# Kernel optimization log

Measured on AMD Instinct MI355X. Metric: run time of the kernel, lower is better.

The kernel has to match this reference:

```python
import jax, jax.numpy as jnp
import numpy as np

N, T, n, C, C2 = 4, 8, 16384, 64, 64

def setup_inputs() -> dict:
    key = jax.random.key(0)
    k1, k2, k3, k4, k5 = jax.random.split(key, 5)
    return {
        "key_mem": jax.random.normal(k1, (N, T, n, C), dtype=jnp.float32),
        "val_mem": jax.random.normal(k2, (N, T, n, C2), dtype=jnp.float32),
        "key_cur": jax.random.normal(k3, (N, n, C), dtype=jnp.float32),
        "val_cur": jax.random.normal(k4, (N, n, C2), dtype=jnp.float32),
        "alpha": jax.random.normal(k5, (1,), dtype=jnp.float32),
    }

def reference(key_mem, val_mem, key_cur, val_cur, alpha):
    # kv_mul: contract memory tokens (T*n) -> (N, C, C2), tiny matrix
    kv_mul = jnp.einsum('btnc,btnd->bcd', key_mem, val_mem)
    # softmax over the C axis (dim=1 in torch layout (N, C, C2))
    kv_mul = jax.nn.softmax(kv_mul, axis=1)
    # out: (N, n, C) @ (N, C, C2) -> (N, n, C2)
    out = jnp.einsum('bnc,bcd->bnd', key_cur, kv_mul)
    return alpha * out + val_cur
```

## Files before the change

kernel.cpp:

```cpp
#include <hip/hip_runtime.h>
#include <math.h>

#define N_TOK   16384
#define K_TOT   (8 * N_TOK)
#define N_BATCH 4
#define BPB     128
#define RPB     (K_TOT / BPB)
#define CHUNK   64
#define NCH     (RPB / CHUNK)
#define PITCH_U 34
#define PART_U  (64 * PITCH_U)

typedef short short8 __attribute__((ext_vector_type(8)));
typedef float f32x4  __attribute__((ext_vector_type(4)));

union FragU { uint4 u; short8 s; };

__device__ __forceinline__ uint bf16_rne(float f, float* rounded) {
  uint u = __float_as_uint(f);
  uint r = u + 0x7FFFu + ((u >> 16) & 1u);
  *rounded = __uint_as_float(r & 0xFFFF0000u);
  return r >> 16;
}

__device__ __forceinline__ void barrier_nodrain() {
  asm volatile("" ::: "memory");
  __builtin_amdgcn_s_waitcnt(0xC07F);
  __builtin_amdgcn_s_barrier();
  asm volatile("" ::: "memory");
}

__global__ __launch_bounds__(512, 2) void k1_mfma(
    const float* __restrict__ key, const float* __restrict__ val,
    float* __restrict__ part) {
  __shared__ uint lds[2][4 * PART_U];

  int blk  = blockIdx.x;
  int b    = blk / BPB;
  int p    = blk % BPB;
  int t    = threadIdx.x;
  int wave = t >> 6;
  int lane = t & 63;

  int arr = t >> 8;
  int tt  = t & 255;
  int c0  = (tt & 15) * 4;
  int r0  = (tt >> 4) * 4;
  const float* src = arr ? val : key;
  size_t rowbase = (size_t)b * K_TOT + (size_t)p * RPB;
  uint sbase = arr * 2 * PART_U;

  int mt  = wave >> 1;
  int ntb = (wave & 1) * 2;
  int m16 = lane & 15;
  int ko  = lane >> 4;

  f32x4 acc[2] = {{0.f, 0.f, 0.f, 0.f}, {0.f, 0.f, 0.f, 0.f}};
  float4 ld[2][4];

  auto load_chunk = [&](int ch, int par) {
#pragma unroll
    for (int q = 0; q < 4; q++)
      ld[par][q] =
          *(const float4*)&src[(rowbase + (size_t)ch * CHUNK + r0 + q) * 64 + c0];
  };

  auto write_chunk = [&](int par) {
#pragma unroll
    for (int cc = 0; cc < 4; cc++) {
      uint h[4], l[4];
#pragma unroll
      for (int q = 0; q < 4; q++) {
        float f = (&ld[par][q].x)[cc];
        float hf;
        h[q] = bf16_rne(f, &hf);
        float dummy;
        l[q] = bf16_rne(f - hf, &dummy);
      }
      uint2 hp = make_uint2(h[0] | (h[1] << 16), h[2] | (h[3] << 16));
      uint2 lp = make_uint2(l[0] | (l[1] << 16), l[2] | (l[3] << 16));
      uint base = sbase + (uint)(c0 + cc) * PITCH_U + (uint)(r0 >> 1);
      *(uint2*)&lds[par][base]          = hp;
      *(uint2*)&lds[par][base + PART_U] = lp;
    }
  };

  auto frag = [&](uint idx) {
    FragU F;
    uint2 a0 = *(const uint2*)&lds[0][0];
    (void)a0;
    uint2 lo = *(const uint2*)&((&lds[0][0])[idx]);
    uint2 hi = *(const uint2*)&((&lds[0][0])[idx + 2]);
    F.u = make_uint4(lo.x, lo.y, hi.x, hi.y);
    return F;
  };

  auto compute = [&](int par) {
    const uint* L = &lds[par][0];
#pragma unroll
    for (int ks = 0; ks < 2; ks++) {
      uint ao = (uint)(mt * 16 + m16) * PITCH_U + ks * 16 + ko * 4;
      FragU Ah, Al;
      {
        uint2 lo = *(const uint2*)&L[ao];
        uint2 hi = *(const uint2*)&L[ao + 2];
        Ah.u = make_uint4(lo.x, lo.y, hi.x, hi.y);
      }
      {
        uint2 lo = *(const uint2*)&L[ao + PART_U];
        uint2 hi = *(const uint2*)&L[ao + PART_U + 2];
        Al.u = make_uint4(lo.x, lo.y, hi.x, hi.y);
      }
#pragma unroll
      for (int nn = 0; nn < 2; nn++) {
        uint bo = 2 * PART_U + (uint)((ntb + nn) * 16 + m16) * PITCH_U +
                  ks * 16 + ko * 4;
        FragU Bh, Bl;
        {
          uint2 lo = *(const uint2*)&L[bo];
          uint2 hi = *(const uint2*)&L[bo + 2];
          Bh.u = make_uint4(lo.x, lo.y, hi.x, hi.y);
        }
        {
          uint2 lo = *(const uint2*)&L[bo + PART_U];
          uint2 hi = *(const uint2*)&L[bo + PART_U + 2];
          Bl.u = make_uint4(lo.x, lo.y, hi.x, hi.y);
        }
        acc[nn] = __builtin_amdgcn_mfma_f32_16x16x32_bf16(Ah.s, Bh.s, acc[nn], 0, 0, 0);
        acc[nn] = __builtin_amdgcn_mfma_f32_16x16x32_bf16(Ah.s, Bl.s, acc[nn], 0, 0, 0);
        acc[nn] = __builtin_amdgcn_mfma_f32_16x16x32_bf16(Al.s, Bh.s, acc[nn], 0, 0, 0);
      }
    }
  };

  load_chunk(0, 0);
  load_chunk(1, 1);
  write_chunk(0);
  barrier_nodrain();

#pragma unroll
  for (int ch = 0; ch < NCH; ch++) {
    if (ch + 2 < NCH) load_chunk(ch + 2, ch & 1);
    compute(ch & 1);
    if (ch + 1 < NCH) write_chunk((ch + 1) & 1);
    barrier_nodrain();
  }

  float* dst = part + (size_t)blk * 4096;
#pragma unroll
  for (int nn = 0; nn < 2; nn++) {
    int d = (ntb + nn) * 16 + m16;
#pragma unroll
    for (int r = 0; r < 4; r++) {
      int c = mt * 16 + ko * 4 + r;
      dst[c * 64 + d] = acc[nn][r];
    }
  }
}

__global__ __launch_bounds__(256, 4) void k2_reduce(
    const float* __restrict__ part, float* __restrict__ kv, int bpb) {
  int b  = blockIdx.x >> 6;
  int c  = blockIdx.x & 63;
  int p4 = threadIdx.x >> 6;
  int d  = threadIdx.x & 63;

  float s = 0.f;
  int iters = bpb >> 2;
  const float* src = part + (size_t)(b * bpb) * 4096 + c * 64 + d;
#pragma unroll 4
  for (int x = 0; x < iters; x++) s += src[(size_t)(p4 + 4 * x) * 4096];

  __shared__ float l[256];
  l[threadIdx.x] = s;
  __syncthreads();
  if (p4 == 0)
    kv[((size_t)b * 64 + c) * 64 + d] = l[d] + l[64 + d] + l[128 + d] + l[192 + d];
}

__global__ __launch_bounds__(256, 4) void k3_out(
    const float* __restrict__ kv, const float* __restrict__ keyc,
    const float* __restrict__ valc, const float* __restrict__ alphap,
    float* __restrict__ out) {
  __shared__ float Ps[4096];
  __shared__ float kT[64 * 68];
  __shared__ float redm[4][64];
  __shared__ float reds[4][64];

  int bb = blockIdx.x >> 8;
  int mb = blockIdx.x & 255;
  int m0 = mb * 64;
  int t = threadIdx.x;

  int d  = t & 63;
  int cg = t >> 6;
  const float* kvb = kv + (size_t)bb * 4096;
  float v[16];
  float mx = -3.0e38f;
#pragma unroll
  for (int i = 0; i < 16; i++) {
    v[i] = kvb[(cg * 16 + i) * 64 + d];
    mx = fmaxf(mx, v[i]);
  }
  redm[cg][d] = mx;

  int r  = t >> 2;
  int cb = (t & 3) * 16;
  const float* krow = keyc + ((size_t)bb * N_TOK + m0 + r) * 64;
#pragma unroll
  for (int u = 0; u < 4; u++) {
    float4 kk = *(const float4*)&krow[cb + 4 * u];
    int c = cb + 4 * u;
    kT[(c + 0) * 68 + r] = kk.x;
    kT[(c + 1) * 68 + r] = kk.y;
    kT[(c + 2) * 68 + r] = kk.z;
    kT[(c + 3) * 68 + r] = kk.w;
  }
  __syncthreads();

  mx = fmaxf(fmaxf(redm[0][d], redm[1][d]), fmaxf(redm[2][d], redm[3][d]));
  float s = 0.f;
#pragma unroll
  for (int i = 0; i < 16; i++) {
    float e = __expf(v[i] - mx);
    Ps[(cg * 16 + i) * 64 + d] = e;
    s += e;
  }
  reds[cg][d] = s;
  __syncthreads();

  int wave = t >> 6, lane = t & 63;
  int mi = lane >> 3, j = lane & 7;
  int m = wave * 16 + mi * 2;

  float acc[2][8];
#pragma unroll
  for (int a = 0; a < 2; a++)
#pragma unroll
    for (int dd = 0; dd < 8; dd++) acc[a][dd] = 0.f;

#pragma unroll 4
  for (int c = 0; c < 64; c++) {
    float2 kk = *(const float2*)&kT[c * 68 + m];
    float4 p0 = *(const float4*)&Ps[c * 64 + 8 * j];
    float4 p1 = *(const float4*)&Ps[c * 64 + 8 * j + 4];
    float pr[8] = {p0.x, p0.y, p0.z, p0.w, p1.x, p1.y, p1.z, p1.w};
#pragma unroll
    for (int dd = 0; dd < 8; dd++) {
      acc[0][dd] = fmaf(kk.x, pr[dd], acc[0][dd]);
      acc[1][dd] = fmaf(kk.y, pr[dd], acc[1][dd]);
    }
  }

  float alpha = alphap[0];
  float sc[8];
#pragma unroll
  for (int dd = 0; dd < 8; dd++) {
    int dq = 8 * j + dd;
    float den = reds[0][dq] + reds[1][dq] + reds[2][dq] + reds[3][dq];
    sc[dd] = alpha / den;
  }

#pragma unroll
  for (int a = 0; a < 2; a++) {
    size_t off = ((size_t)bb * N_TOK + m0 + m + a) * 64 + 8 * j;
    float4 v0 = *(const float4*)&valc[off];
    float4 v1 = *(const float4*)&valc[off + 4];
    float4 o0 = make_float4(fmaf(sc[0], acc[a][0], v0.x),
                            fmaf(sc[1], acc[a][1], v0.y),
                            fmaf(sc[2], acc[a][2], v0.z),
                            fmaf(sc[3], acc[a][3], v0.w));
    float4 o1 = make_float4(fmaf(sc[4], acc[a][4], v1.x),
                            fmaf(sc[5], acc[a][5], v1.y),
                            fmaf(sc[6], acc[a][6], v1.z),
                            fmaf(sc[7], acc[a][7], v1.w));
    *(float4*)&out[off] = o0;
    *(float4*)&out[off + 4] = o1;
  }
}

extern "C" void kernel_launch(void* const* d_in, const int* in_sizes, int n_in,
                              void* d_out, int out_size, void* d_ws,
                              size_t ws_size, hipStream_t stream) {
  const float* key_mem = (const float*)d_in[0];
  const float* val_mem = (const float*)d_in[1];
  const float* key_cur = (const float*)d_in[2];
  const float* val_cur = (const float*)d_in[3];
  const float* alpha   = (const float*)d_in[4];
  float* out = (float*)d_out;
  float* ws  = (float*)d_ws;

  float* part = ws;
  float* kv   = ws + (size_t)(N_BATCH * BPB) * 4096;

  k1_mfma<<<N_BATCH * BPB, 512, 0, stream>>>(key_mem, val_mem, part);
  k2_reduce<<<256, 256, 0, stream>>>(part, kv, BPB);
  k3_out<<<N_BATCH * (N_TOK / 64), 256, 0, stream>>>(kv, key_cur, val_cur,
                                                     alpha, out);
}
```

Before: 314.9 us.

## Replace split-bf16 MFMA reduction with fp32 FMA outer products fed by direct global-to-LDS loads

The first kernel stops converting key/value chunks to hi/lo bf16 pairs and running three MFMAs per tile. It now stages raw fp32 chunks straight into LDS with global_load_lds and accumulates 4x4 outer products with scalar FMAs, with the two half-blocks combined through LDS at the end. This drops the register round-trip and conversion work and gives exact fp32 accumulation, but moves the math from matrix cores to vector ALUs. The pipeline also shrinks from two chunks in flight to one.

```diff
diff --git a/kernel.cpp b/kernel.cpp
--- a/kernel.cpp
+++ b/kernel.cpp
@@ -8,32 +8,23 @@
 #define RPB     (K_TOT / BPB)
 #define CHUNK   64
 #define NCH     (RPB / CHUNK)
-#define PITCH_U 34
-#define PART_U  (64 * PITCH_U)
-
-typedef short short8 __attribute__((ext_vector_type(8)));
-typedef float f32x4  __attribute__((ext_vector_type(4)));
-
-union FragU { uint4 u; short8 s; };
-
-__device__ __forceinline__ uint bf16_rne(float f, float* rounded) {
-  uint u = __float_as_uint(f);
-  uint r = u + 0x7FFFu + ((u >> 16) & 1u);
-  *rounded = __uint_as_float(r & 0xFFFF0000u);
-  return r >> 16;
-}
-
-__device__ __forceinline__ void barrier_nodrain() {
-  asm volatile("" ::: "memory");
-  __builtin_amdgcn_s_waitcnt(0xC07F);
-  __builtin_amdgcn_s_barrier();
-  asm volatile("" ::: "memory");
-}
-
-__global__ __launch_bounds__(512, 2) void k1_mfma(
+
+
+typedef float f32x4 __attribute__((ext_vector_type(4)));
+
+__device__ __forceinline__ void gload16(const float* g, float* l) {
+  __builtin_amdgcn_global_load_lds(
+      (const __attribute__((address_space(1))) void*)g,
+      (__attribute__((address_space(3))) void*)l, 16, 0, 0);
+}
+
+#define WAIT_VM0   0x0F70u
+#define WAIT_LGKM0 0xC07Fu
+
+__global__ __launch_bounds__(512, 2) void k1_outer(
     const float* __restrict__ key, const float* __restrict__ val,
     float* __restrict__ part) {
-  __shared__ uint lds[2][4 * PART_U];
+  __shared__ float lds[2][8192];
 
   int blk  = blockIdx.x;
   int b    = blk / BPB;
@@ -42,118 +33,82 @@
   int wave = t >> 6;
   int lane = t & 63;
 
-  int arr = t >> 8;
-  int tt  = t & 255;
-  int c0  = (tt & 15) * 4;
-  int r0  = (tt >> 4) * 4;
-  const float* src = arr ? val : key;
-  size_t rowbase = (size_t)b * K_TOT + (size_t)p * RPB;
-  uint sbase = arr * 2 * PART_U;
-
-  int mt  = wave >> 1;
-  int ntb = (wave & 1) * 2;
-  int m16 = lane & 15;
-  int ko  = lane >> 4;
-
-  f32x4 acc[2] = {{0.f, 0.f, 0.f, 0.f}, {0.f, 0.f, 0.f, 0.f}};
-  float4 ld[2][4];
-
-  auto load_chunk = [&](int ch, int par) {
+  size_t base = ((size_t)b * K_TOT + (size_t)p * RPB) * 64;
+
+  const float* sarr = (wave < 4) ? (key + base) : (val + base);
+  uint ldsarr = (wave < 4) ? 0u : 4096u;
+  uint uoff   = (uint)((wave & 3) * 1024);
+
+  int half = t >> 8;
+  int tid  = t & 255;
+  int c4   = tid >> 4;
+  int d4   = tid & 15;
+  int r0   = half * 32;
+
+  float acc[4][4];
+#pragma unroll
+  for (int i = 0; i < 4; i++)
+#pragma unroll
+    for (int j = 0; j < 4; j++) acc[i][j] = 0.f;
+
+  auto stage = [&](int ch, int par) {
+    const float* g = sarr + (size_t)ch * (CHUNK * 64) + uoff + lane * 4;
+    float* l = &lds[par][ldsarr + uoff];
 #pragma unroll
     for (int q = 0; q < 4; q++)
-      ld[par][q] =
-          *(const float4*)&src[(rowbase + (size_t)ch * CHUNK + r0 + q) * 64 + c0];
+      gload16(g + q * 256, l + q * 256);
   };
 
-  auto write_chunk = [&](int par) {
-#pragma unroll
-    for (int cc = 0; cc < 4; cc++) {
-      uint h[4], l[4];
-#pragma unroll
-      for (int q = 0; q < 4; q++) {
-        float f = (&ld[par][q].x)[cc];
-        float hf;
-        h[q] = bf16_rne(f, &hf);
-        float dummy;
-        l[q] = bf16_rne(f - hf, &dummy);
-      }
-      uint2 hp = make_uint2(h[0] | (h[1] << 16), h[2] | (h[3] << 16));
-      uint2 lp = make_uint2(l[0] | (l[1] << 16), l[2] | (l[3] << 16));
-      uint base = sbase + (uint)(c0 + cc) * PITCH_U + (uint)(r0 >> 1);
-      *(uint2*)&lds[par][base]          = hp;
-      *(uint2*)&lds[par][base + PART_U] = lp;
+  auto compute = [&](int par) {
+    const float* Kb = &lds[par][(r0 << 6) + c4 * 4];
+    const float* Vb = &lds[par][4096 + (r0 << 6) + d4 * 4];
+#pragma unroll
+    for (int r = 0; r < 32; r++) {
+      float4 kk = *(const float4*)&Kb[r * 64];
+      float4 vv = *(const float4*)&Vb[r * 64];
+#pragma unroll
+      for (int i = 0; i < 4; i++)
+#pragma unroll
+        for (int j = 0; j < 4; j++)
+          acc[i][j] = fmaf((&kk.x)[i], (&vv.x)[j], acc[i][j]);
     }
   };
 
-  auto frag = [&](uint idx) {
-    FragU F;
-    uint2 a0 = *(const uint2*)&lds[0][0];
-    (void)a0;
-    uint2 lo = *(const uint2*)&((&lds[0][0])[idx]);
-    uint2 hi = *(const uint2*)&((&lds[0][0])[idx + 2]);
-    F.u = make_uint4(lo.x, lo.y, hi.x, hi.y);
-    return F;
-  };
-
-  auto compute = [&](int par) {
-    const uint* L = &lds[par][0];
-#pragma unroll
-    for (int ks = 0; ks < 2; ks++) {
-      uint ao = (uint)(mt * 16 + m16) * PITCH_U + ks * 16 + ko * 4;
-      FragU Ah, Al;
-      {
-        uint2 lo = *(const uint2*)&L[ao];
-        uint2 hi = *(const uint2*)&L[ao + 2];
-        Ah.u = make_uint4(lo.x, lo.y, hi.x, hi.y);
-      }
-      {
-        uint2 lo = *(const uint2*)&L[ao + PART_U];
-        uint2 hi = *(const uint2*)&L[ao + PART_U + 2];
-        Al.u = make_uint4(lo.x, lo.y, hi.x, hi.y);
-      }
-#pragma unroll
-      for (int nn = 0; nn < 2; nn++) {
-        uint bo = 2 * PART_U + (uint)((ntb + nn) * 16 + m16) * PITCH_U +
-                  ks * 16 + ko * 4;
-        FragU Bh, Bl;
-        {
-          uint2 lo = *(const uint2*)&L[bo];
-          uint2 hi = *(const uint2*)&L[bo + 2];
-          Bh.u = make_uint4(lo.x, lo.y, hi.x, hi.y);
-        }
-        {
-          uint2 lo = *(const uint2*)&L[bo + PART_U];
-          uint2 hi = *(const uint2*)&L[bo + PART_U + 2];
-          Bl.u = make_uint4(lo.x, lo.y, hi.x, hi.y);
-        }
-        acc[nn] = __builtin_amdgcn_mfma_f32_16x16x32_bf16(Ah.s, Bh.s, acc[nn], 0, 0, 0);
-        acc[nn] = __builtin_amdgcn_mfma_f32_16x16x32_bf16(Ah.s, Bl.s, acc[nn], 0, 0, 0);
-        acc[nn] = __builtin_amdgcn_mfma_f32_16x16x32_bf16(Al.s, Bh.s, acc[nn], 0, 0, 0);
-      }
-    }
-  };
-
-  load_chunk(0, 0);
-  load_chunk(1, 1);
-  write_chunk(0);
-  barrier_nodrain();
-
-#pragma unroll
+  stage(0, 0);
+  asm volatile("" ::: "memory");
+  __builtin_amdgcn_s_waitcnt(WAIT_VM0);
+  __builtin_amdgcn_s_barrier();
+  asm volatile("" ::: "memory");
+
+#pragma unroll 2
   for (int ch = 0; ch < NCH; ch++) {
-    if (ch + 2 < NCH) load_chunk(ch + 2, ch & 1);
+    if (ch + 1 < NCH) stage(ch + 1, (ch + 1) & 1);
     compute(ch & 1);
-    if (ch + 1 < NCH) write_chunk((ch + 1) & 1);
-    barrier_nodrain();
-  }
-
-  float* dst = part + (size_t)blk * 4096;
-#pragma unroll
-  for (int nn = 0; nn < 2; nn++) {
-    int d = (ntb + nn) * 16 + m16;
-#pragma unroll
-    for (int r = 0; r < 4; r++) {
-      int c = mt * 16 + ko * 4 + r;
-      dst[c * 64 + d] = acc[nn][r];
+    asm volatile("" ::: "memory");
+    __builtin_amdgcn_s_waitcnt(WAIT_VM0);
+    __builtin_amdgcn_s_barrier();
+    asm volatile("" ::: "memory");
+  }
+
+  float* scratch = &lds[0][0];
+  if (half) {
+#pragma unroll
+    for (int i = 0; i < 4; i++)
+      *(float4*)&scratch[tid * 20 + i * 4] =
+          make_float4(acc[i][0], acc[i][1], acc[i][2], acc[i][3]);
+  }
+  asm volatile("" ::: "memory");
+  __builtin_amdgcn_s_waitcnt(WAIT_LGKM0);
+  __builtin_amdgcn_s_barrier();
+  asm volatile("" ::: "memory");
+  if (!half) {
+    float* dst = part + (size_t)blk * 4096;
+#pragma unroll
+    for (int i = 0; i < 4; i++) {
+      float4 s = *(const float4*)&scratch[tid * 20 + i * 4];
+      float4 o = make_float4(acc[i][0] + s.x, acc[i][1] + s.y,
+                             acc[i][2] + s.z, acc[i][3] + s.w);
+      *(float4*)&dst[(c4 * 4 + i) * 64 + d4 * 4] = o;
     }
   }
 }
@@ -293,7 +248,7 @@
   float* part = ws;
   float* kv   = ws + (size_t)(N_BATCH * BPB) * 4096;
 
-  k1_mfma<<<N_BATCH * BPB, 512, 0, stream>>>(key_mem, val_mem, part);
+  k1_outer<<<N_BATCH * BPB, 512, 0, stream>>>(key_mem, val_mem, part);
   k2_reduce<<<256, 256, 0, stream>>>(part, kv, BPB);
   k3_out<<<N_BATCH * (N_TOK / 64), 256, 0, stream>>>(kv, key_cur, val_cur,
                                                      alpha, out);
```

Result: slower. 357.6 us (+13.6%).
